# Kernel tuning notes

Hardware: AMD Instinct MI355X
Metric: run time of the kernel (lower is better)

Reference implementation:

```python
import jax, jax.numpy as jnp
import numpy as np

B, C, G = 512, 65536, 4096
EPS = 1e-5


def setup_inputs() -> dict:
    key = jax.random.key(0)
    k1, k2 = jax.random.split(key)
    x = jax.random.normal(k1, (B, C), dtype=jnp.float32)
    channel_groups = jax.random.randint(k2, (C,), 0, G, dtype=jnp.int64)
    gamma = jnp.ones((G,), dtype=jnp.float32)
    beta = jnp.zeros((G,), dtype=jnp.float32)
    return {"x": x, "channel_groups": channel_groups, "gamma": gamma, "beta": beta}


def reference(x, channel_groups, gamma, beta):
    # x: (B, C). Group stats computed over the full batch AND all channels in a group.
    # Since every row shares the same channel->group mapping, reduce over batch first
    # (a dense sum), then do a single segment reduction over C -- same math as the
    # original scatter-mean over B*C flattened elements.
    cg = channel_groups
    ones_c = jnp.ones((C,), dtype=x.dtype)
    # elements per group = B * (channels in group)
    counts = jax.ops.segment_sum(ones_c, cg, num_segments=G) * x.shape[0]
    counts = jnp.maximum(counts, 1.0)
    s1 = jax.ops.segment_sum(jnp.sum(x, axis=0), cg, num_segments=G)          # [G]
    s2 = jax.ops.segment_sum(jnp.sum(x * x, axis=0), cg, num_segments=G)      # [G]
    mean = s1 / counts
    var = s2 / counts - mean * mean  # E[(x-mean)^2] == E[x^2] - mean^2 (biased, matches scatter-mean)
    inv = 1.0 / jnp.sqrt(var + EPS)
    # gather per-channel stats, broadcast over batch
    normed = (x - mean[cg]) * inv[cg]
    normed = normed * gamma[cg] + beta[cg]
    return normed[:, :, None]  # (B, C, 1)
```

## Files before the change

### kernel.cpp

```cpp
#include <hip/hip_runtime.h>


constexpr int B = 512;
constexpr int C = 65536;
constexpr int G = 4096;
constexpr int SPLIT = 16;
constexpr int ROWS = B / SPLIT;
#define EPS 1e-5f

constexpr int SCRATCH_N = 4 * C + 5 * G;
__device__ float g_scr[SCRATCH_N];

#define CSUM   (g_scr)
#define CSUM2  (g_scr + C)
#define GSUM   (g_scr + 2 * C)
#define GSUM2  (g_scr + 2 * C + G)
#define GCNT   (g_scr + 2 * C + 2 * G)
#define GSCALE (g_scr + 2 * C + 3 * G)
#define GSHIFT (g_scr + 2 * C + 4 * G)
#define CSCALE (g_scr + 2 * C + 5 * G)
#define CSHIFT (g_scr + 3 * C + 5 * G)

__global__ __launch_bounds__(256) void zero_k() {
    int i = blockIdx.x * 256 + threadIdx.x;
    if (i < 2 * C + 3 * G) g_scr[i] = 0.0f;
}

__global__ __launch_bounds__(256) void colsum_k(const float* __restrict__ x) {
    const int nblk_c = C / 1024;
    const int c4 = (blockIdx.x % nblk_c) * 256 + threadIdx.x;
    const int chunk = blockIdx.x / nblk_c;
    const float4* __restrict__ xp =
        (const float4*)(x + (size_t)chunk * ROWS * C) + c4;
    float4 s = {0.f, 0.f, 0.f, 0.f};
    float4 s2 = {0.f, 0.f, 0.f, 0.f};
#pragma unroll 4
    for (int r = 0; r < ROWS; ++r) {
        float4 v = xp[(size_t)r * (C / 4)];
        s.x += v.x; s.y += v.y; s.z += v.z; s.w += v.w;
        s2.x = fmaf(v.x, v.x, s2.x);
        s2.y = fmaf(v.y, v.y, s2.y);
        s2.z = fmaf(v.z, v.z, s2.z);
        s2.w = fmaf(v.w, v.w, s2.w);
    }
    const int c = c4 * 4;
    atomicAdd(&CSUM[c + 0], s.x);
    atomicAdd(&CSUM[c + 1], s.y);
    atomicAdd(&CSUM[c + 2], s.z);
    atomicAdd(&CSUM[c + 3], s.w);
    atomicAdd(&CSUM2[c + 0], s2.x);
    atomicAdd(&CSUM2[c + 1], s2.y);
    atomicAdd(&CSUM2[c + 2], s2.z);
    atomicAdd(&CSUM2[c + 3], s2.w);
}

__global__ __launch_bounds__(256) void gscatter_k(const int* __restrict__ cg) {
    const int c = blockIdx.x * 256 + threadIdx.x;
    const int g = cg[c];
    atomicAdd(&GSUM[g], CSUM[c]);
    atomicAdd(&GSUM2[g], CSUM2[c]);
    atomicAdd(&GCNT[g], 1.0f);
}

__global__ __launch_bounds__(256) void finalize_k(const float* __restrict__ gamma,
                                                  const float* __restrict__ beta) {
    const int g = blockIdx.x * 256 + threadIdx.x;
    if (g < G) {
        float cnt = fmaxf(GCNT[g] * (float)B, 1.0f);
        float mean = GSUM[g] / cnt;
        float var = GSUM2[g] / cnt - mean * mean;
        float inv = 1.0f / sqrtf(var + EPS);
        float sc = gamma[g] * inv;
        GSCALE[g] = sc;
        GSHIFT[g] = fmaf(-mean, sc, beta[g]);
    }
}

__global__ __launch_bounds__(256) void cgather_k(const int* __restrict__ cg) {
    const int c = blockIdx.x * 256 + threadIdx.x;
    const int g = cg[c];
    CSCALE[c] = GSCALE[g];
    CSHIFT[c] = GSHIFT[g];
}

__global__ __launch_bounds__(256) void norm_k(const float* __restrict__ x,
                                              float* __restrict__ out) {
    const float4* __restrict__ x4 = (const float4*)x;
    const float4* __restrict__ sc4 = (const float4*)CSCALE;
    const float4* __restrict__ sh4 = (const float4*)CSHIFT;
    float4* __restrict__ o4 = (float4*)out;
    const size_t n4 = (size_t)B * C / 4;
    const size_t stride = (size_t)gridDim.x * blockDim.x;
    for (size_t i = (size_t)blockIdx.x * blockDim.x + threadIdx.x; i < n4; i += stride) {
        const int c4 = (int)(i & (C / 4 - 1));
        float4 xv = x4[i];
        float4 s = sc4[c4];
        float4 t = sh4[c4];
        float4 o;
        o.x = fmaf(xv.x, s.x, t.x);
        o.y = fmaf(xv.y, s.y, t.y);
        o.z = fmaf(xv.z, s.z, t.z);
        o.w = fmaf(xv.w, s.w, t.w);
        o4[i] = o;
    }
}

extern "C" void kernel_launch(void* const* d_in, const int* in_sizes, int n_in,
                              void* d_out, int out_size, void* d_ws, size_t ws_size,
                              hipStream_t stream) {
    const float* x = (const float*)d_in[0];
    const int* cg = (const int*)d_in[1];
    const float* gamma = (const float*)d_in[2];
    const float* beta = (const float*)d_in[3];
    float* out = (float*)d_out;
    (void)d_ws; (void)ws_size; (void)in_sizes; (void)n_in; (void)out_size;

    constexpr int nzero = 2 * C + 3 * G;
    zero_k<<<(nzero + 255) / 256, 256, 0, stream>>>();
    colsum_k<<<(C / 1024) * SPLIT, 256, 0, stream>>>(x);
    gscatter_k<<<C / 256, 256, 0, stream>>>(cg);
    finalize_k<<<G / 256, 256, 0, stream>>>(gamma, beta);
    cgather_k<<<C / 256, 256, 0, stream>>>(cg);
    norm_k<<<4096, 256, 0, stream>>>(x, out);
}
```

Before: 314.1 us.

## Replace column-sum atomics with partial buffers and fuse finalize into per-channel gather

```diff
diff --git a/kernel.cpp b/kernel.cpp
--- a/kernel.cpp
+++ b/kernel.cpp
@@ -4,26 +4,26 @@
 constexpr int B = 512;
 constexpr int C = 65536;
 constexpr int G = 4096;
-constexpr int SPLIT = 16;
+constexpr int SPLIT = 32;
 constexpr int ROWS = B / SPLIT;
+constexpr int BATCH = 8;
 #define EPS 1e-5f
 
-constexpr int SCRATCH_N = 4 * C + 5 * G;
-__device__ float g_scr[SCRATCH_N];
-
-#define CSUM   (g_scr)
-#define CSUM2  (g_scr + C)
-#define GSUM   (g_scr + 2 * C)
-#define GSUM2  (g_scr + 2 * C + G)
-#define GCNT   (g_scr + 2 * C + 2 * G)
-#define GSCALE (g_scr + 2 * C + 3 * G)
-#define GSHIFT (g_scr + 2 * C + 4 * G)
-#define CSCALE (g_scr + 2 * C + 5 * G)
-#define CSHIFT (g_scr + 3 * C + 5 * G)
+__device__ float g_part1[SPLIT * C];
+__device__ float g_part2[SPLIT * C];
+__device__ float g_gsum[G];
+__device__ float g_gsum2[G];
+__device__ float g_gcnt[G];
+__device__ float g_cscale[C];
+__device__ float g_cshift[C];
 
 __global__ __launch_bounds__(256) void zero_k() {
     int i = blockIdx.x * 256 + threadIdx.x;
-    if (i < 2 * C + 3 * G) g_scr[i] = 0.0f;
+    if (i < G) {
+        g_gsum[i] = 0.0f;
+        g_gsum2[i] = 0.0f;
+        g_gcnt[i] = 0.0f;
+    }
 }
 
 __global__ __launch_bounds__(256) void colsum_k(const float* __restrict__ x) {
@@ -34,75 +34,66 @@
         (const float4*)(x + (size_t)chunk * ROWS * C) + c4;
     float4 s = {0.f, 0.f, 0.f, 0.f};
     float4 s2 = {0.f, 0.f, 0.f, 0.f};
-#pragma unroll 4
-    for (int r = 0; r < ROWS; ++r) {
-        float4 v = xp[(size_t)r * (C / 4)];
-        s.x += v.x; s.y += v.y; s.z += v.z; s.w += v.w;
-        s2.x = fmaf(v.x, v.x, s2.x);
-        s2.y = fmaf(v.y, v.y, s2.y);
-        s2.z = fmaf(v.z, v.z, s2.z);
-        s2.w = fmaf(v.w, v.w, s2.w);
+    float4 vbuf[BATCH];
+    for (int base = 0; base < ROWS; base += BATCH) {
+#pragma unroll
+        for (int j = 0; j < BATCH; ++j)
+            vbuf[j] = xp[(size_t)(base + j) * (C / 4)];
+#pragma unroll
+        for (int j = 0; j < BATCH; ++j) {
+            float4 v = vbuf[j];
+            s.x += v.x; s.y += v.y; s.z += v.z; s.w += v.w;
+            s2.x = fmaf(v.x, v.x, s2.x);
+            s2.y = fmaf(v.y, v.y, s2.y);
+            s2.z = fmaf(v.z, v.z, s2.z);
+            s2.w = fmaf(v.w, v.w, s2.w);
+        }
     }
-    const int c = c4 * 4;
-    atomicAdd(&CSUM[c + 0], s.x);
-    atomicAdd(&CSUM[c + 1], s.y);
-    atomicAdd(&CSUM[c + 2], s.z);
-    atomicAdd(&CSUM[c + 3], s.w);
-    atomicAdd(&CSUM2[c + 0], s2.x);
-    atomicAdd(&CSUM2[c + 1], s2.y);
-    atomicAdd(&CSUM2[c + 2], s2.z);
-    atomicAdd(&CSUM2[c + 3], s2.w);
+    ((float4*)g_part1)[(size_t)chunk * (C / 4) + c4] = s;
+    ((float4*)g_part2)[(size_t)chunk * (C / 4) + c4] = s2;
 }
 
-__global__ __launch_bounds__(256) void gscatter_k(const int* __restrict__ cg) {
+__global__ __launch_bounds__(256) void gsum_k(const int* __restrict__ cg) {
+    const int c = blockIdx.x * 256 + threadIdx.x;
+    float s = 0.f, s2 = 0.f;
+#pragma unroll 8
+    for (int k = 0; k < SPLIT; ++k) {
+        s += g_part1[(size_t)k * C + c];
+        s2 += g_part2[(size_t)k * C + c];
+    }
+    const int g = cg[c];
+    atomicAdd(&g_gsum[g], s);
+    atomicAdd(&g_gsum2[g], s2);
+    atomicAdd(&g_gcnt[g], 1.0f);
+}
+
+__global__ __launch_bounds__(256) void cfinal_k(const int* __restrict__ cg,
+                                                const float* __restrict__ gamma,
+                                                const float* __restrict__ beta) {
     const int c = blockIdx.x * 256 + threadIdx.x;
     const int g = cg[c];
-    atomicAdd(&GSUM[g], CSUM[c]);
-    atomicAdd(&GSUM2[g], CSUM2[c]);
-    atomicAdd(&GCNT[g], 1.0f);
-}
-
-__global__ __launch_bounds__(256) void finalize_k(const float* __restrict__ gamma,
-                                                  const float* __restrict__ beta) {
-    const int g = blockIdx.x * 256 + threadIdx.x;
-    if (g < G) {
-        float cnt = fmaxf(GCNT[g] * (float)B, 1.0f);
-        float mean = GSUM[g] / cnt;
-        float var = GSUM2[g] / cnt - mean * mean;
-        float inv = 1.0f / sqrtf(var + EPS);
-        float sc = gamma[g] * inv;
-        GSCALE[g] = sc;
-        GSHIFT[g] = fmaf(-mean, sc, beta[g]);
-    }
-}
-
-__global__ __launch_bounds__(256) void cgather_k(const int* __restrict__ cg) {
-    const int c = blockIdx.x * 256 + threadIdx.x;
-    const int g = cg[c];
-    CSCALE[c] = GSCALE[g];
-    CSHIFT[c] = GSHIFT[g];
+    float cnt = fmaxf(g_gcnt[g] * (float)B, 1.0f);
+    float mean = g_gsum[g] / cnt;
+    float var = g_gsum2[g] / cnt - mean * mean;
+    float inv = 1.0f / sqrtf(var + EPS);
+    float sc = gamma[g] * inv;
+    g_cscale[c] = sc;
+    g_cshift[c] = fmaf(-mean, sc, beta[g]);
 }
 
 __global__ __launch_bounds__(256) void norm_k(const float* __restrict__ x,
                                               float* __restrict__ out) {
-    const float4* __restrict__ x4 = (const float4*)x;
-    const float4* __restrict__ sc4 = (const float4*)CSCALE;
-    const float4* __restrict__ sh4 = (const float4*)CSHIFT;
-    float4* __restrict__ o4 = (float4*)out;
-    const size_t n4 = (size_t)B * C / 4;
-    const size_t stride = (size_t)gridDim.x * blockDim.x;
-    for (size_t i = (size_t)blockIdx.x * blockDim.x + threadIdx.x; i < n4; i += stride) {
-        const int c4 = (int)(i & (C / 4 - 1));
-        float4 xv = x4[i];
-        float4 s = sc4[c4];
-        float4 t = sh4[c4];
-        float4 o;
-        o.x = fmaf(xv.x, s.x, t.x);
-        o.y = fmaf(xv.y, s.y, t.y);
-        o.z = fmaf(xv.z, s.z, t.z);
-        o.w = fmaf(xv.w, s.w, t.w);
-        o4[i] = o;
-    }
+    const size_t i = (size_t)blockIdx.x * 256 + threadIdx.x;
+    const int c4 = (int)(i & (C / 4 - 1));
+    float4 xv = ((const float4*)x)[i];
+    float4 s = ((const float4*)g_cscale)[c4];
+    float4 t = ((const float4*)g_cshift)[c4];
+    float4 o;
+    o.x = fmaf(xv.x, s.x, t.x);
+    o.y = fmaf(xv.y, s.y, t.y);
+    o.z = fmaf(xv.z, s.z, t.z);
+    o.w = fmaf(xv.w, s.w, t.w);
+    ((float4*)out)[i] = o;
 }
 
 extern "C" void kernel_launch(void* const* d_in, const int* in_sizes, int n_in,
@@ -115,11 +106,9 @@
     float* out = (float*)d_out;
     (void)d_ws; (void)ws_size; (void)in_sizes; (void)n_in; (void)out_size;
 
-    constexpr int nzero = 2 * C + 3 * G;
-    zero_k<<<(nzero + 255) / 256, 256, 0, stream>>>();
+    zero_k<<<(G + 255) / 256, 256, 0, stream>>>();
     colsum_k<<<(C / 1024) * SPLIT, 256, 0, stream>>>(x);
-    gscatter_k<<<C / 256, 256, 0, stream>>>(cg);
-    finalize_k<<<G / 256, 256, 0, stream>>>(gamma, beta);
-    cgather_k<<<C / 256, 256, 0, stream>>>(cg);
-    norm_k<<<4096, 256, 0, stream>>>(x, out);
+    gsum_k<<<C / 256, 256, 0, stream>>>(cg);
+    cfinal_k<<<C / 256, 256, 0, stream>>>(cg, gamma, beta);
+    norm_k<<<(B * C / 4) / 256, 256, 0, stream>>>(x, out);
 }
```

Result: faster. 272.8 us (-13.1%).
